# Optimization experiments

Hardware: AMD Instinct MI355X
Metric: run time of the kernel (lower is better)

The kernel has to match this reference:

```python
import jax, jax.numpy as jnp
import numpy as np

TOP_K = 2


def setup_inputs() -> dict:
    key = jax.random.key(0)
    k1, k2 = jax.random.split(key)
    x = jax.random.normal(k1, (4, 4096, 2048), dtype=jnp.float32)
    W = jax.random.normal(k2, (64, 2048), dtype=jnp.float32) * (1.0 / np.sqrt(2048))
    return {"x": x, "W": W}


def reference(x, W):
    B, S, D = x.shape
    E = W.shape[0]
    # logits: [B*S, E] via linear router (no bias)
    flat = x.reshape(-1, D)
    logits = jnp.einsum('td,ed->te', flat, W)
    probs = jax.nn.softmax(logits, axis=-1)
    # eval path: top-k indices
    _, top_k_indices = jax.lax.top_k(probs, TOP_K)          # [T, K]
    # scatter 1s -> mask; scatter gathered probs -> router_probs (== probs*mask)
    router_mask = jax.nn.one_hot(top_k_indices, E, dtype=probs.dtype).sum(axis=-2)  # [T, E]
    router_probs = probs * router_mask
    # normalize (top_k > 1: gradient flows through the sum)
    router_probs = router_probs / router_probs.sum(axis=-1, keepdims=True)
    return (router_mask.reshape(B, S, E),
            top_k_indices.reshape(B, S, TOP_K),
            router_probs.reshape(B, S, E),
            probs.reshape(B, S, E))
```

## Files before the change

kernel.cpp:

```cpp
#include <hip/hip_runtime.h>
#include <math.h>


#define D_DIM 2048
#define E_DIM 64

typedef __bf16 bf16x8 __attribute__((ext_vector_type(8)));
typedef unsigned short us8 __attribute__((ext_vector_type(8)));
typedef float f32x4 __attribute__((ext_vector_type(4)));

static __device__ __forceinline__ unsigned short f2bf(float f) {
    unsigned int u = __float_as_uint(f);
    u += 0x7fffu + ((u >> 16) & 1u);
    return (unsigned short)(u >> 16);
}
static __device__ __forceinline__ float bf2f(unsigned short h) {
    return __uint_as_float(((unsigned int)h) << 16);
}
static __device__ __forceinline__ void split4(const float4 v, ushort4* h, ushort4* l) {
    h->x = f2bf(v.x); l->x = f2bf(v.x - bf2f(h->x));
    h->y = f2bf(v.y); l->y = f2bf(v.y - bf2f(h->y));
    h->z = f2bf(v.z); l->z = f2bf(v.z - bf2f(h->z));
    h->w = f2bf(v.w); l->w = f2bf(v.w - bf2f(h->w));
}

static __device__ __forceinline__ void gld_lds16(const void* g, void* l) {
    __builtin_amdgcn_global_load_lds(
        (const __attribute__((address_space(1))) unsigned int*)g,
        (__attribute__((address_space(3))) unsigned int*)l,
        16, 0, 0);
}

__global__ __launch_bounds__(256, 1) void convert_w(
    const float4* __restrict__ W4, unsigned short* __restrict__ WH,
    unsigned short* __restrict__ WL)
{
    int i = blockIdx.x * 256 + threadIdx.x;
    float4 v = W4[i];
    ushort4 h, l;
    split4(v, &h, &l);
    *(ushort4*)&WH[i * 4] = h;
    *(ushort4*)&WL[i * 4] = l;
}

__global__ __launch_bounds__(256, 1) void router_fused(
    const float* __restrict__ x,
    const unsigned short* __restrict__ WHg, const unsigned short* __restrict__ WLg,
    float* __restrict__ mask_out, float* __restrict__ idx_out,
    float* __restrict__ rp_out, float* __restrict__ probs_out)
{
    __shared__ __align__(16) float          XF [2][64 * 64];
    __shared__ __align__(16) unsigned short WHs[2][64 * 64];
    __shared__ __align__(16) unsigned short WLs[2][64 * 64];

    const int tid  = threadIdx.x;
    const int lane = tid & 63;
    const int wv   = tid >> 6;
    const int quad = lane >> 4;
    const int l16  = lane & 15;

    const int t0  = blockIdx.x << 6;
    const int NCH = D_DIM >> 6;

    f32x4 acc[4];
    #pragma unroll
    for (int n = 0; n < 4; ++n) { f32x4 z = {0.f, 0.f, 0.f, 0.f}; acc[n] = z; }

    const int srow = wv * 4 + (lane >> 4);
    const int scg  = lane & 15;
    const int we   = wv * 8 + (lane >> 3);
    const int wo   = lane & 7;

    {
        #pragma unroll
        for (int i = 0; i < 4; ++i) {
            int row = i * 16 + srow;
            int cg  = scg ^ (row & 15);
            gld_lds16(x + (size_t)(t0 + row) * D_DIM + cg * 4,
                      &XF[0][(i * 256 + wv * 64) * 4]);
        }
        #pragma unroll
        for (int i2 = 0; i2 < 2; ++i2) {
            int e  = i2 * 32 + we;
            int og = wo ^ (e & 7);
            gld_lds16(WHg + (size_t)e * D_DIM + og * 8,
                      &WHs[0][(i2 * 256 + wv * 64) * 8]);
            gld_lds16(WLg + (size_t)e * D_DIM + og * 8,
                      &WLs[0][(i2 * 256 + wv * 64) * 8]);
        }
    }
    __syncthreads();

    int buf = 0;
    for (int ch = 0; ch < NCH; ++ch) {
        if (ch + 1 < NCH) {
            const int kc = (ch + 1) << 6;
            const int nb = buf ^ 1;
            #pragma unroll
            for (int i = 0; i < 4; ++i) {
                int row = i * 16 + srow;
                int cg  = scg ^ (row & 15);
                gld_lds16(x + (size_t)(t0 + row) * D_DIM + kc + cg * 4,
                          &XF[nb][(i * 256 + wv * 64) * 4]);
            }
            #pragma unroll
            for (int i2 = 0; i2 < 2; ++i2) {
                int e  = i2 * 32 + we;
                int og = wo ^ (e & 7);
                gld_lds16(WHg + (size_t)e * D_DIM + kc + og * 8,
                          &WHs[nb][(i2 * 256 + wv * 64) * 8]);
                gld_lds16(WLg + (size_t)e * D_DIM + kc + og * 8,
                          &WLs[nb][(i2 * 256 + wv * 64) * 8]);
            }
        }

        #pragma unroll
        for (int ks = 0; ks < 2; ++ks) {
            const int tr = wv * 16 + l16;
            const int c0 = ks * 8 + quad * 2;
            float4 xa = *(const float4*)&XF[buf][(tr * 16 + ( c0      ^ (tr & 15))) * 4];
            float4 xb = *(const float4*)&XF[buf][(tr * 16 + ((c0 + 1) ^ (tr & 15))) * 4];
            ushort4 h0, l0, h1, l1;
            split4(xa, &h0, &l0);
            split4(xb, &h1, &l1);
            union { us8 u; bf16x8 b; } ua, ul;
            ua.u = (us8){h0.x, h0.y, h0.z, h0.w, h1.x, h1.y, h1.z, h1.w};
            ul.u = (us8){l0.x, l0.y, l0.z, l0.w, l1.x, l1.y, l1.z, l1.w};

            #pragma unroll
            for (int n = 0; n < 4; ++n) {
                int e = n * 16 + l16;
                int o = ks * 4 + quad;
                int s = e * 8 + (o ^ (e & 7));
                bf16x8 bh = *(const bf16x8*)&WHs[buf][s * 8];
                bf16x8 bl = *(const bf16x8*)&WLs[buf][s * 8];
                acc[n] = __builtin_amdgcn_mfma_f32_16x16x32_bf16(ua.b, bh, acc[n], 0, 0, 0);
                acc[n] = __builtin_amdgcn_mfma_f32_16x16x32_bf16(ul.b, bh, acc[n], 0, 0, 0);
                acc[n] = __builtin_amdgcn_mfma_f32_16x16x32_bf16(ua.b, bl, acc[n], 0, 0, 0);
            }
        }
        __syncthreads();
        buf ^= 1;
    }

    #pragma unroll
    for (int r = 0; r < 4; ++r) {
        const int t = t0 + wv * 16 + quad * 4 + r;
        const float v0 = acc[0][r], v1 = acc[1][r], v2 = acc[2][r], v3 = acc[3][r];

        float bv = v0; int bi = l16;
        if (v1 > bv) { bv = v1; bi = 16 + l16; }
        if (v2 > bv) { bv = v2; bi = 32 + l16; }
        if (v3 > bv) { bv = v3; bi = 48 + l16; }
        #pragma unroll
        for (int off = 1; off < 16; off <<= 1) {
            float ov = __shfl_xor(bv, off);
            int   oi = __shfl_xor(bi, off);
            bool take = (ov > bv) || (ov == bv && oi < bi);
            bv = take ? ov : bv;
            bi = take ? oi : bi;
        }
        const float m = bv; const int i1 = bi;

        const float p0 = __expf(v0 - m), p1 = __expf(v1 - m);
        const float p2 = __expf(v2 - m), p3 = __expf(v3 - m);
        float s = p0 + p1 + p2 + p3;
        #pragma unroll
        for (int off = 1; off < 16; off <<= 1) s += __shfl_xor(s, off);

        const float w0 = (i1 == l16)      ? -INFINITY : v0;
        const float w1 = (i1 == 16 + l16) ? -INFINITY : v1;
        const float w2 = (i1 == 32 + l16) ? -INFINITY : v2;
        const float w3 = (i1 == 48 + l16) ? -INFINITY : v3;
        float cv = w0; int ci = l16;
        if (w1 > cv) { cv = w1; ci = 16 + l16; }
        if (w2 > cv) { cv = w2; ci = 32 + l16; }
        if (w3 > cv) { cv = w3; ci = 48 + l16; }
        #pragma unroll
        for (int off = 1; off < 16; off <<= 1) {
            float ov = __shfl_xor(cv, off);
            int   oi = __shfl_xor(ci, off);
            bool take = (ov > cv) || (ov == cv && oi < ci);
            cv = take ? ov : cv;
            ci = take ? oi : ci;
        }
        const int i2 = ci;

        const float inv_s = 1.f / s;
        const float q0 = p0 * inv_s, q1 = p1 * inv_s;
        const float q2 = p2 * inv_s, q3 = p3 * inv_s;
        const bool m0 = (l16 == i1)      || (l16 == i2);
        const bool m1 = (16 + l16 == i1) || (16 + l16 == i2);
        const bool m2 = (32 + l16 == i1) || (32 + l16 == i2);
        const bool m3 = (48 + l16 == i1) || (48 + l16 == i2);

        float pd = (m0 ? q0 : 0.f) + (m1 ? q1 : 0.f)
                 + (m2 ? q2 : 0.f) + (m3 ? q3 : 0.f);
        #pragma unroll
        for (int off = 1; off < 16; off <<= 1) pd += __shfl_xor(pd, off);
        const float ipd = 1.f / pd;

        const size_t base = (size_t)t * 64 + l16;
        probs_out[base]      = q0;
        probs_out[base + 16] = q1;
        probs_out[base + 32] = q2;
        probs_out[base + 48] = q3;
        mask_out[base]      = m0 ? 1.f : 0.f;
        mask_out[base + 16] = m1 ? 1.f : 0.f;
        mask_out[base + 32] = m2 ? 1.f : 0.f;
        mask_out[base + 48] = m3 ? 1.f : 0.f;
        rp_out[base]      = m0 ? q0 * ipd : 0.f;
        rp_out[base + 16] = m1 ? q1 * ipd : 0.f;
        rp_out[base + 32] = m2 ? q2 * ipd : 0.f;
        rp_out[base + 48] = m3 ? q3 * ipd : 0.f;
        if (l16 == 0) {
            idx_out[(size_t)t * 2]     = (float)i1;
            idx_out[(size_t)t * 2 + 1] = (float)i2;
        }
    }
}

extern "C" void kernel_launch(void* const* d_in, const int* in_sizes, int n_in,
                              void* d_out, int out_size, void* d_ws, size_t ws_size,
                              hipStream_t stream) {
    const float* x = (const float*)d_in[0];
    const float* W = (const float*)d_in[1];
    float* out = (float*)d_out;

    const int T  = in_sizes[0] / D_DIM;
    const int WN = in_sizes[1];

    unsigned short* WH = (unsigned short*)d_ws;
    unsigned short* WL = WH + WN;

    float* mask_out  = out;
    float* idx_out   = out + (size_t)T * E_DIM;
    float* rp_out    = idx_out + (size_t)T * 2;
    float* probs_out = rp_out + (size_t)T * E_DIM;

    convert_w<<<dim3(WN / 1024), dim3(256), 0, stream>>>((const float4*)W, WH, WL);
    router_fused<<<dim3(T / 64), dim3(256), 0, stream>>>(
        x, WH, WL, mask_out, idx_out, rp_out, probs_out);
}
```

Measured before the change: 225.9 us.

## Replace LDS-staged GEMM with direct register loads, one wave per 16 tokens

Drops the shared-memory double buffering and the barriers. Each single-wave block now handles 16 tokens and loads x and the bf16 hi/lo weight fragments straight from global memory into registers, keeping a 4-deep software prefetch. This removes LDS traffic and synchronisation and raises the block count for occupancy. In exchange, every wave re-reads the full W from global/L2 (4x more W traffic per token than before), and register pressure rises from holding four staged fragment sets.

```diff
diff --git a/kernel.cpp b/kernel.cpp
--- a/kernel.cpp
+++ b/kernel.cpp
@@ -22,13 +22,6 @@
     h->y = f2bf(v.y); l->y = f2bf(v.y - bf2f(h->y));
     h->z = f2bf(v.z); l->z = f2bf(v.z - bf2f(h->z));
     h->w = f2bf(v.w); l->w = f2bf(v.w - bf2f(h->w));
-}
-
-static __device__ __forceinline__ void gld_lds16(const void* g, void* l) {
-    __builtin_amdgcn_global_load_lds(
-        (const __attribute__((address_space(1))) unsigned int*)g,
-        (__attribute__((address_space(3))) unsigned int*)l,
-        16, 0, 0);
 }
 
 __global__ __launch_bounds__(256, 1) void convert_w(
@@ -43,109 +36,86 @@
     *(ushort4*)&WL[i * 4] = l;
 }
 
-__global__ __launch_bounds__(256, 1) void router_fused(
+struct XS { float4 a, b; };
+struct WS { bf16x8 h0, h1, h2, h3, l0, l1, l2, l3; };
+
+static __device__ __forceinline__ void ldx(XS& s, const float* p) {
+    s.a = *(const float4*)(p);
+    s.b = *(const float4*)(p + 4);
+}
+static __device__ __forceinline__ void ldw(WS& s, const unsigned short* ph,
+                                           const unsigned short* pl) {
+    s.h0 = *(const bf16x8*)(ph);
+    s.h1 = *(const bf16x8*)(ph + 16 * D_DIM);
+    s.h2 = *(const bf16x8*)(ph + 32 * D_DIM);
+    s.h3 = *(const bf16x8*)(ph + 48 * D_DIM);
+    s.l0 = *(const bf16x8*)(pl);
+    s.l1 = *(const bf16x8*)(pl + 16 * D_DIM);
+    s.l2 = *(const bf16x8*)(pl + 32 * D_DIM);
+    s.l3 = *(const bf16x8*)(pl + 48 * D_DIM);
+}
+
+static __device__ __forceinline__ void comp(const XS& xv, const WS& w, f32x4* acc) {
+    ushort4 h0, l0, h1, l1;
+    split4(xv.a, &h0, &l0);
+    split4(xv.b, &h1, &l1);
+    union { us8 u; bf16x8 b; } ua, ul;
+    ua.u = (us8){h0.x, h0.y, h0.z, h0.w, h1.x, h1.y, h1.z, h1.w};
+    ul.u = (us8){l0.x, l0.y, l0.z, l0.w, l1.x, l1.y, l1.z, l1.w};
+    acc[0] = __builtin_amdgcn_mfma_f32_16x16x32_bf16(ua.b, w.h0, acc[0], 0, 0, 0);
+    acc[0] = __builtin_amdgcn_mfma_f32_16x16x32_bf16(ul.b, w.h0, acc[0], 0, 0, 0);
+    acc[0] = __builtin_amdgcn_mfma_f32_16x16x32_bf16(ua.b, w.l0, acc[0], 0, 0, 0);
+    acc[1] = __builtin_amdgcn_mfma_f32_16x16x32_bf16(ua.b, w.h1, acc[1], 0, 0, 0);
+    acc[1] = __builtin_amdgcn_mfma_f32_16x16x32_bf16(ul.b, w.h1, acc[1], 0, 0, 0);
+    acc[1] = __builtin_amdgcn_mfma_f32_16x16x32_bf16(ua.b, w.l1, acc[1], 0, 0, 0);
+    acc[2] = __builtin_amdgcn_mfma_f32_16x16x32_bf16(ua.b, w.h2, acc[2], 0, 0, 0);
+    acc[2] = __builtin_amdgcn_mfma_f32_16x16x32_bf16(ul.b, w.h2, acc[2], 0, 0, 0);
+    acc[2] = __builtin_amdgcn_mfma_f32_16x16x32_bf16(ua.b, w.l2, acc[2], 0, 0, 0);
+    acc[3] = __builtin_amdgcn_mfma_f32_16x16x32_bf16(ua.b, w.h3, acc[3], 0, 0, 0);
+    acc[3] = __builtin_amdgcn_mfma_f32_16x16x32_bf16(ul.b, w.h3, acc[3], 0, 0, 0);
+    acc[3] = __builtin_amdgcn_mfma_f32_16x16x32_bf16(ua.b, w.l3, acc[3], 0, 0, 0);
+}
+
+__global__ __launch_bounds__(64, 1) void router_fused(
     const float* __restrict__ x,
     const unsigned short* __restrict__ WHg, const unsigned short* __restrict__ WLg,
     float* __restrict__ mask_out, float* __restrict__ idx_out,
     float* __restrict__ rp_out, float* __restrict__ probs_out)
 {
-    __shared__ __align__(16) float          XF [2][64 * 64];
-    __shared__ __align__(16) unsigned short WHs[2][64 * 64];
-    __shared__ __align__(16) unsigned short WLs[2][64 * 64];
-
-    const int tid  = threadIdx.x;
-    const int lane = tid & 63;
-    const int wv   = tid >> 6;
+    const int lane = threadIdx.x;
     const int quad = lane >> 4;
     const int l16  = lane & 15;
-
-    const int t0  = blockIdx.x << 6;
-    const int NCH = D_DIM >> 6;
+    const int t0   = blockIdx.x << 4;
+
+    const float*          xp  = x   + (size_t)(t0 + l16) * D_DIM + quad * 8;
+    const unsigned short* whp = WHg + (size_t)l16 * D_DIM + quad * 8;
+    const unsigned short* wlp = WLg + (size_t)l16 * D_DIM + quad * 8;
 
     f32x4 acc[4];
     #pragma unroll
     for (int n = 0; n < 4; ++n) { f32x4 z = {0.f, 0.f, 0.f, 0.f}; acc[n] = z; }
 
-    const int srow = wv * 4 + (lane >> 4);
-    const int scg  = lane & 15;
-    const int we   = wv * 8 + (lane >> 3);
-    const int wo   = lane & 7;
-
-    {
-        #pragma unroll
-        for (int i = 0; i < 4; ++i) {
-            int row = i * 16 + srow;
-            int cg  = scg ^ (row & 15);
-            gld_lds16(x + (size_t)(t0 + row) * D_DIM + cg * 4,
-                      &XF[0][(i * 256 + wv * 64) * 4]);
-        }
-        #pragma unroll
-        for (int i2 = 0; i2 < 2; ++i2) {
-            int e  = i2 * 32 + we;
-            int og = wo ^ (e & 7);
-            gld_lds16(WHg + (size_t)e * D_DIM + og * 8,
-                      &WHs[0][(i2 * 256 + wv * 64) * 8]);
-            gld_lds16(WLg + (size_t)e * D_DIM + og * 8,
-                      &WLs[0][(i2 * 256 + wv * 64) * 8]);
-        }
-    }
-    __syncthreads();
-
-    int buf = 0;
-    for (int ch = 0; ch < NCH; ++ch) {
-        if (ch + 1 < NCH) {
-            const int kc = (ch + 1) << 6;
-            const int nb = buf ^ 1;
-            #pragma unroll
-            for (int i = 0; i < 4; ++i) {
-                int row = i * 16 + srow;
-                int cg  = scg ^ (row & 15);
-                gld_lds16(x + (size_t)(t0 + row) * D_DIM + kc + cg * 4,
-                          &XF[nb][(i * 256 + wv * 64) * 4]);
-            }
-            #pragma unroll
-            for (int i2 = 0; i2 < 2; ++i2) {
-                int e  = i2 * 32 + we;
-                int og = wo ^ (e & 7);
-                gld_lds16(WHg + (size_t)e * D_DIM + kc + og * 8,
-                          &WHs[nb][(i2 * 256 + wv * 64) * 8]);
-                gld_lds16(WLg + (size_t)e * D_DIM + kc + og * 8,
-                          &WLs[nb][(i2 * 256 + wv * 64) * 8]);
-            }
-        }
-
-        #pragma unroll
-        for (int ks = 0; ks < 2; ++ks) {
-            const int tr = wv * 16 + l16;
-            const int c0 = ks * 8 + quad * 2;
-            float4 xa = *(const float4*)&XF[buf][(tr * 16 + ( c0      ^ (tr & 15))) * 4];
-            float4 xb = *(const float4*)&XF[buf][(tr * 16 + ((c0 + 1) ^ (tr & 15))) * 4];
-            ushort4 h0, l0, h1, l1;
-            split4(xa, &h0, &l0);
-            split4(xb, &h1, &l1);
-            union { us8 u; bf16x8 b; } ua, ul;
-            ua.u = (us8){h0.x, h0.y, h0.z, h0.w, h1.x, h1.y, h1.z, h1.w};
-            ul.u = (us8){l0.x, l0.y, l0.z, l0.w, l1.x, l1.y, l1.z, l1.w};
-
-            #pragma unroll
-            for (int n = 0; n < 4; ++n) {
-                int e = n * 16 + l16;
-                int o = ks * 4 + quad;
-                int s = e * 8 + (o ^ (e & 7));
-                bf16x8 bh = *(const bf16x8*)&WHs[buf][s * 8];
-                bf16x8 bl = *(const bf16x8*)&WLs[buf][s * 8];
-                acc[n] = __builtin_amdgcn_mfma_f32_16x16x32_bf16(ua.b, bh, acc[n], 0, 0, 0);
-                acc[n] = __builtin_amdgcn_mfma_f32_16x16x32_bf16(ul.b, bh, acc[n], 0, 0, 0);
-                acc[n] = __builtin_amdgcn_mfma_f32_16x16x32_bf16(ua.b, bl, acc[n], 0, 0, 0);
-            }
-        }
-        __syncthreads();
-        buf ^= 1;
+    XS x0, x1, x2, x3;
+    WS w0, w1, w2, w3;
+    ldx(x0, xp +  0); ldw(w0, whp +  0, wlp +  0);
+    ldx(x1, xp + 32); ldw(w1, whp + 32, wlp + 32);
+    ldx(x2, xp + 64); ldw(w2, whp + 64, wlp + 64);
+    ldx(x3, xp + 96); ldw(w3, whp + 96, wlp + 96);
+
+    for (int jb = 0; jb < 64; jb += 4) {
+        const int p4 = min(jb + 4, 63) << 5;
+        const int p5 = min(jb + 5, 63) << 5;
+        const int p6 = min(jb + 6, 63) << 5;
+        const int p7 = min(jb + 7, 63) << 5;
+        comp(x0, w0, acc); ldx(x0, xp + p4); ldw(w0, whp + p4, wlp + p4);
+        comp(x1, w1, acc); ldx(x1, xp + p5); ldw(w1, whp + p5, wlp + p5);
+        comp(x2, w2, acc); ldx(x2, xp + p6); ldw(w2, whp + p6, wlp + p6);
+        comp(x3, w3, acc); ldx(x3, xp + p7); ldw(w3, whp + p7, wlp + p7);
     }
 
     #pragma unroll
     for (int r = 0; r < 4; ++r) {
-        const int t = t0 + wv * 16 + quad * 4 + r;
+        const int t = t0 + quad * 4 + r;
         const float v0 = acc[0][r], v1 = acc[1][r], v2 = acc[2][r], v3 = acc[3][r];
 
         float bv = v0; int bi = l16;
@@ -168,14 +138,14 @@
         #pragma unroll
         for (int off = 1; off < 16; off <<= 1) s += __shfl_xor(s, off);
 
-        const float w0 = (i1 == l16)      ? -INFINITY : v0;
-        const float w1 = (i1 == 16 + l16) ? -INFINITY : v1;
-        const float w2 = (i1 == 32 + l16) ? -INFINITY : v2;
-        const float w3 = (i1 == 48 + l16) ? -INFINITY : v3;
-        float cv = w0; int ci = l16;
-        if (w1 > cv) { cv = w1; ci = 16 + l16; }
-        if (w2 > cv) { cv = w2; ci = 32 + l16; }
-        if (w3 > cv) { cv = w3; ci = 48 + l16; }
+        const float u0 = (i1 == l16)      ? -INFINITY : v0;
+        const float u1 = (i1 == 16 + l16) ? -INFINITY : v1;
+        const float u2 = (i1 == 32 + l16) ? -INFINITY : v2;
+        const float u3 = (i1 == 48 + l16) ? -INFINITY : v3;
+        float cv = u0; int ci = l16;
+        if (u1 > cv) { cv = u1; ci = 16 + l16; }
+        if (u2 > cv) { cv = u2; ci = 32 + l16; }
+        if (u3 > cv) { cv = u3; ci = 48 + l16; }
         #pragma unroll
         for (int off = 1; off < 16; off <<= 1) {
             float ov = __shfl_xor(cv, off);
@@ -239,6 +209,6 @@
     float* probs_out = rp_out + (size_t)T * E_DIM;
 
     convert_w<<<dim3(WN / 1024), dim3(256), 0, stream>>>((const float4*)W, WH, WL);
-    router_fused<<<dim3(T / 64), dim3(256), 0, stream>>>(
+    router_fused<<<dim3(T / 16), dim3(64), 0, stream>>>(
         x, WH, WL, mask_out, idx_out, rp_out, probs_out);
 }
```

Result: slower. 289.1 us (+28.0%).

## Shrink token tile to 16 per block, split experts across waves, LDS epilogue

Applied to the files above, without the earlier changes.

Each block now handles 16 tokens instead of 64, with each of the four waves computing one 16-expert slice of the logits. That quadruples the grid and raises the occupancy hint to 4 blocks per CU. The epilogue stages the logits through LDS so that one wave handles one token row at a time. Softmax, top-2 and the output stores then use full 64-lane reductions with coalesced row writes. In exchange, every block reloads the full W tiles for only 16 tokens, so W traffic through L2 per token rises fourfold.

```diff
diff --git a/kernel.cpp b/kernel.cpp
--- a/kernel.cpp
+++ b/kernel.cpp
@@ -43,13 +43,13 @@
     *(ushort4*)&WL[i * 4] = l;
 }
 
-__global__ __launch_bounds__(256, 1) void router_fused(
+__global__ __launch_bounds__(256, 4) void router_fused(
     const float* __restrict__ x,
     const unsigned short* __restrict__ WHg, const unsigned short* __restrict__ WLg,
     float* __restrict__ mask_out, float* __restrict__ idx_out,
     float* __restrict__ rp_out, float* __restrict__ probs_out)
 {
-    __shared__ __align__(16) float          XF [2][64 * 64];
+    __shared__ __align__(16) float          XF [2][16 * 64];
     __shared__ __align__(16) unsigned short WHs[2][64 * 64];
     __shared__ __align__(16) unsigned short WLs[2][64 * 64];
 
@@ -59,26 +59,19 @@
     const int quad = lane >> 4;
     const int l16  = lane & 15;
 
-    const int t0  = blockIdx.x << 6;
+    const int t0  = blockIdx.x << 4;
     const int NCH = D_DIM >> 6;
 
-    f32x4 acc[4];
-    #pragma unroll
-    for (int n = 0; n < 4; ++n) { f32x4 z = {0.f, 0.f, 0.f, 0.f}; acc[n] = z; }
-
-    const int srow = wv * 4 + (lane >> 4);
-    const int scg  = lane & 15;
+    f32x4 acc = {0.f, 0.f, 0.f, 0.f};
+
+    const int xrow = tid >> 4;
+    const int xcg  = (tid & 15) ^ (xrow & 15);
     const int we   = wv * 8 + (lane >> 3);
     const int wo   = lane & 7;
 
     {
-        #pragma unroll
-        for (int i = 0; i < 4; ++i) {
-            int row = i * 16 + srow;
-            int cg  = scg ^ (row & 15);
-            gld_lds16(x + (size_t)(t0 + row) * D_DIM + cg * 4,
-                      &XF[0][(i * 256 + wv * 64) * 4]);
-        }
+        gld_lds16(x + (size_t)(t0 + xrow) * D_DIM + xcg * 4,
+                  &XF[0][(wv * 64) * 4]);
         #pragma unroll
         for (int i2 = 0; i2 < 2; ++i2) {
             int e  = i2 * 32 + we;
@@ -96,13 +89,8 @@
         if (ch + 1 < NCH) {
             const int kc = (ch + 1) << 6;
             const int nb = buf ^ 1;
-            #pragma unroll
-            for (int i = 0; i < 4; ++i) {
-                int row = i * 16 + srow;
-                int cg  = scg ^ (row & 15);
-                gld_lds16(x + (size_t)(t0 + row) * D_DIM + kc + cg * 4,
-                          &XF[nb][(i * 256 + wv * 64) * 4]);
-            }
+            gld_lds16(x + (size_t)(t0 + xrow) * D_DIM + kc + xcg * 4,
+                      &XF[nb][(wv * 64) * 4]);
             #pragma unroll
             for (int i2 = 0; i2 < 2; ++i2) {
                 int e  = i2 * 32 + we;
@@ -116,7 +104,7 @@
 
         #pragma unroll
         for (int ks = 0; ks < 2; ++ks) {
-            const int tr = wv * 16 + l16;
+            const int tr = l16;
             const int c0 = ks * 8 + quad * 2;
             float4 xa = *(const float4*)&XF[buf][(tr * 16 + ( c0      ^ (tr & 15))) * 4];
             float4 xb = *(const float4*)&XF[buf][(tr * 16 + ((c0 + 1) ^ (tr & 15))) * 4];
@@ -127,93 +115,67 @@
             ua.u = (us8){h0.x, h0.y, h0.z, h0.w, h1.x, h1.y, h1.z, h1.w};
             ul.u = (us8){l0.x, l0.y, l0.z, l0.w, l1.x, l1.y, l1.z, l1.w};
 
-            #pragma unroll
-            for (int n = 0; n < 4; ++n) {
-                int e = n * 16 + l16;
-                int o = ks * 4 + quad;
-                int s = e * 8 + (o ^ (e & 7));
-                bf16x8 bh = *(const bf16x8*)&WHs[buf][s * 8];
-                bf16x8 bl = *(const bf16x8*)&WLs[buf][s * 8];
-                acc[n] = __builtin_amdgcn_mfma_f32_16x16x32_bf16(ua.b, bh, acc[n], 0, 0, 0);
-                acc[n] = __builtin_amdgcn_mfma_f32_16x16x32_bf16(ul.b, bh, acc[n], 0, 0, 0);
-                acc[n] = __builtin_amdgcn_mfma_f32_16x16x32_bf16(ua.b, bl, acc[n], 0, 0, 0);
-            }
+            const int e = wv * 16 + l16;
+            const int o = ks * 4 + quad;
+            const int s = e * 8 + (o ^ (e & 7));
+            bf16x8 bh = *(const bf16x8*)&WHs[buf][s * 8];
+            bf16x8 bl = *(const bf16x8*)&WLs[buf][s * 8];
+            acc = __builtin_amdgcn_mfma_f32_16x16x32_bf16(ua.b, bh, acc, 0, 0, 0);
+            acc = __builtin_amdgcn_mfma_f32_16x16x32_bf16(ul.b, bh, acc, 0, 0, 0);
+            acc = __builtin_amdgcn_mfma_f32_16x16x32_bf16(ua.b, bl, acc, 0, 0, 0);
         }
         __syncthreads();
         buf ^= 1;
     }
 
+    float* L = &XF[0][0];
     #pragma unroll
-    for (int r = 0; r < 4; ++r) {
-        const int t = t0 + wv * 16 + quad * 4 + r;
-        const float v0 = acc[0][r], v1 = acc[1][r], v2 = acc[2][r], v3 = acc[3][r];
-
-        float bv = v0; int bi = l16;
-        if (v1 > bv) { bv = v1; bi = 16 + l16; }
-        if (v2 > bv) { bv = v2; bi = 32 + l16; }
-        if (v3 > bv) { bv = v3; bi = 48 + l16; }
-        #pragma unroll
-        for (int off = 1; off < 16; off <<= 1) {
-            float ov = __shfl_xor(bv, off);
-            int   oi = __shfl_xor(bi, off);
+    for (int r = 0; r < 4; ++r)
+        L[(quad * 4 + r) * 64 + wv * 16 + l16] = acc[r];
+    __syncthreads();
+
+    for (int i = 0; i < 4; ++i) {
+        const int tl = wv * 4 + i;
+        const int t  = t0 + tl;
+        const float v = L[tl * 64 + lane];
+
+        float bv = v; int bi = lane;
+        #pragma unroll
+        for (int off = 1; off < 64; off <<= 1) {
+            float ov = __shfl_xor(bv, off, 64);
+            int   oi = __shfl_xor(bi, off, 64);
             bool take = (ov > bv) || (ov == bv && oi < bi);
             bv = take ? ov : bv;
             bi = take ? oi : bi;
         }
         const float m = bv; const int i1 = bi;
 
-        const float p0 = __expf(v0 - m), p1 = __expf(v1 - m);
-        const float p2 = __expf(v2 - m), p3 = __expf(v3 - m);
-        float s = p0 + p1 + p2 + p3;
-        #pragma unroll
-        for (int off = 1; off < 16; off <<= 1) s += __shfl_xor(s, off);
-
-        const float w0 = (i1 == l16)      ? -INFINITY : v0;
-        const float w1 = (i1 == 16 + l16) ? -INFINITY : v1;
-        const float w2 = (i1 == 32 + l16) ? -INFINITY : v2;
-        const float w3 = (i1 == 48 + l16) ? -INFINITY : v3;
-        float cv = w0; int ci = l16;
-        if (w1 > cv) { cv = w1; ci = 16 + l16; }
-        if (w2 > cv) { cv = w2; ci = 32 + l16; }
-        if (w3 > cv) { cv = w3; ci = 48 + l16; }
-        #pragma unroll
-        for (int off = 1; off < 16; off <<= 1) {
-            float ov = __shfl_xor(cv, off);
-            int   oi = __shfl_xor(ci, off);
+        const float p = __expf(v - m);
+        float s = p;
+        #pragma unroll
+        for (int off = 1; off < 64; off <<= 1) s += __shfl_xor(s, off, 64);
+        const float prob = p / s;
+
+        const float v2 = (lane == i1) ? -INFINITY : v;
+        float cv = v2; int ci = lane;
+        #pragma unroll
+        for (int off = 1; off < 64; off <<= 1) {
+            float ov = __shfl_xor(cv, off, 64);
+            int   oi = __shfl_xor(ci, off, 64);
             bool take = (ov > cv) || (ov == cv && oi < ci);
             cv = take ? ov : cv;
             ci = take ? oi : ci;
         }
         const int i2 = ci;
 
-        const float inv_s = 1.f / s;
-        const float q0 = p0 * inv_s, q1 = p1 * inv_s;
-        const float q2 = p2 * inv_s, q3 = p3 * inv_s;
-        const bool m0 = (l16 == i1)      || (l16 == i2);
-        const bool m1 = (16 + l16 == i1) || (16 + l16 == i2);
-        const bool m2 = (32 + l16 == i1) || (32 + l16 == i2);
-        const bool m3 = (48 + l16 == i1) || (48 + l16 == i2);
-
-        float pd = (m0 ? q0 : 0.f) + (m1 ? q1 : 0.f)
-                 + (m2 ? q2 : 0.f) + (m3 ? q3 : 0.f);
-        #pragma unroll
-        for (int off = 1; off < 16; off <<= 1) pd += __shfl_xor(pd, off);
-        const float ipd = 1.f / pd;
-
-        const size_t base = (size_t)t * 64 + l16;
-        probs_out[base]      = q0;
-        probs_out[base + 16] = q1;
-        probs_out[base + 32] = q2;
-        probs_out[base + 48] = q3;
-        mask_out[base]      = m0 ? 1.f : 0.f;
-        mask_out[base + 16] = m1 ? 1.f : 0.f;
-        mask_out[base + 32] = m2 ? 1.f : 0.f;
-        mask_out[base + 48] = m3 ? 1.f : 0.f;
-        rp_out[base]      = m0 ? q0 * ipd : 0.f;
-        rp_out[base + 16] = m1 ? q1 * ipd : 0.f;
-        rp_out[base + 32] = m2 ? q2 * ipd : 0.f;
-        rp_out[base + 48] = m3 ? q3 * ipd : 0.f;
-        if (l16 == 0) {
+        const float pd = __shfl(prob, i1, 64) + __shfl(prob, i2, 64);
+        const bool top = (lane == i1) || (lane == i2);
+
+        const size_t base = (size_t)t * 64 + lane;
+        mask_out[base]  = top ? 1.f : 0.f;
+        rp_out[base]    = top ? prob / pd : 0.f;
+        probs_out[base] = prob;
+        if (lane == 0) {
             idx_out[(size_t)t * 2]     = (float)i1;
             idx_out[(size_t)t * 2 + 1] = (float)i2;
         }
@@ -239,6 +201,6 @@
     float* probs_out = rp_out + (size_t)T * E_DIM;
 
     convert_w<<<dim3(WN / 1024), dim3(256), 0, stream>>>((const float4*)W, WH, WL);
-    router_fused<<<dim3(T / 64), dim3(256), 0, stream>>>(
+    router_fused<<<dim3(T / 16), dim3(256), 0, stream>>>(
         x, WH, WL, mask_out, idx_out, rp_out, probs_out);
 }
```

Result: faster. 221.3 us (-2.0%).
